# Performance work log

Hardware: AMD Instinct MI355X
Metric: run time of the kernel (lower is better)

## Reference

```python
import jax, jax.numpy as jnp
import numpy as np

B, S, H, V, T, L = 32, 128, 1024, 32000, 100, 4
SD = 0.02


def setup_inputs() -> dict:
    key = jax.random.key(0)
    ks = jax.random.split(key, 20)
    f = jnp.float32
    return {
        "encoder_outputs": jax.random.normal(ks[0], (B, S, H), f),
        "encoder_hidden": jax.random.normal(ks[1], (L, B, H), f),
        "target_tensor": jax.random.randint(ks[2], (B, T), 0, V, dtype=jnp.int32),
        "emb": jax.random.normal(ks[3], (V, H), f) * SD,
        "w_ih0": jax.random.normal(ks[4], (3 * H, 2 * H), f) * SD,
        "w_hh0": jax.random.normal(ks[5], (3 * H, H), f) * SD,
        "b_ih0": jnp.zeros((3 * H,), f),
        "b_hh0": jnp.zeros((3 * H,), f),
        "w_ih": jax.random.normal(ks[6], (L - 1, 3 * H, H), f) * SD,
        "w_hh": jax.random.normal(ks[7], (L - 1, 3 * H, H), f) * SD,
        "b_ih": jnp.zeros((L - 1, 3 * H), f),
        "b_hh": jnp.zeros((L - 1, 3 * H), f),
        "out_w": jax.random.normal(ks[8], (V, H), f) * SD,
        "out_b": jnp.zeros((V,), f),
        "l1_w": jax.random.normal(ks[9], (3, 2 * H), f) * SD,
        "l1_b": jnp.zeros((3,), f),
        "l2_w": jax.random.normal(ks[10], (1, 3), f) * SD,
        "l2_b": jnp.zeros((1,), f),
    }


def _gru_cell(x, h, w_ih, w_hh, b_ih, b_hh):
    # PyTorch GRUCell math
    gi = x @ w_ih.T + b_ih          # [B, 3H]
    gh = h @ w_hh.T + b_hh          # [B, 3H]
    i_r, i_z, i_n = jnp.split(gi, 3, axis=-1)
    h_r, h_z, h_n = jnp.split(gh, 3, axis=-1)
    r = jax.nn.sigmoid(i_r + h_r)
    z = jax.nn.sigmoid(i_z + h_z)
    n = jnp.tanh(i_n + r * h_n)
    return (1.0 - z) * n + z * h


def reference(encoder_outputs, encoder_hidden, target_tensor, emb,
              w_ih0, w_hh0, b_ih0, b_hh0, w_ih, w_hh, b_ih, b_hh,
              out_w, out_b, l1_w, l1_b, l2_w, l2_b):
    b, h = encoder_hidden.shape[1], encoder_hidden.shape[2]
    enc_h = encoder_hidden[0]  # [B, H] 'updated_encoder_hidden'
    # teacher forcing: step 0 uses input 0, step i uses target[:, i-1]
    inputs = jnp.concatenate(
        [jnp.zeros((b, 1), target_tensor.dtype), target_tensor[:, :T - 1]],
        axis=1).T  # [T, B]

    def step(hidden, inp_t):
        # a[:] = hidden[0][-1] -> broadcast last batch row of layer-0 hidden
        a = jnp.broadcast_to(hidden[0, -1], (b, h))
        enc = jnp.concatenate([a, enc_h], axis=1)          # [B, 2H]
        s = (enc @ l1_w.T + l1_b) @ l2_w.T + l2_b          # [B, 1]
        scores = jax.nn.softmax(s, axis=0)                 # softmax over batch dim
        C = jnp.sum(enc_h * scores, axis=0)                # [H]
        e = jax.nn.relu(emb[inp_t])                        # [B, H]
        x = jnp.concatenate([e, jnp.broadcast_to(C, (b, h))], axis=-1)  # [B, 2H]
        h0 = _gru_cell(x, hidden[0], w_ih0, w_hh0, b_ih0, b_hh0)
        hs = [h0]
        xl = h0
        for l in range(L - 1):
            hl = _gru_cell(xl, hidden[l + 1], w_ih[l], w_hh[l], b_ih[l], b_hh[l])
            hs.append(hl)
            xl = hl
        logits = xl @ out_w.T + out_b                      # [B, V]
        return jnp.stack(hs), (logits, scores)

    hidden_fin, (logits, scores) = jax.lax.scan(step, encoder_hidden, inputs)
    dec_out = jax.nn.log_softmax(jnp.transpose(logits, (1, 0, 2)), axis=-1)  # [B, T, V]
    return dec_out, hidden_fin, scores[-1]
```

## Files before the change

### kernel.cpp

```cpp
#include <hip/hip_runtime.h>
#include <hip/hip_bf16.h>
#include <math.h>

#define B_ 32
#define H_ 1024
#define V_ 32000
#define T_ 100
#define L_ 4
#define TB_ (T_*B_)
#define N3H (3*H_)
#define NBLK 224
#define L0BLK 32
#define FSTRIDE 16

typedef __attribute__((ext_vector_type(8))) short bf16x8;
typedef __attribute__((ext_vector_type(4))) float f32x4;
typedef __attribute__((ext_vector_type(4))) unsigned short u16x4;

__device__ inline unsigned short f2bf(float f) {
    union { float f; unsigned u; } v; v.f = f;
    unsigned r = v.u + 0x7fff + ((v.u >> 16) & 1);
    return (unsigned short)(r >> 16);
}
__device__ inline float bf2f(unsigned short u) {
    union { unsigned u; float f; } v; v.u = ((unsigned)u) << 16; return v.f;
}

__device__ inline bf16x8 ld_h16(const unsigned short* p) {
    union { unsigned long long u[2]; bf16x8 v; } r;
    r.u[0] = __hip_atomic_load((const unsigned long long*)p,
                               __ATOMIC_RELAXED, __HIP_MEMORY_SCOPE_AGENT);
    r.u[1] = __hip_atomic_load((const unsigned long long*)(p + 4),
                               __ATOMIC_RELAXED, __HIP_MEMORY_SCOPE_AGENT);
    return r.v;
}
__device__ inline void st_h2(unsigned short* p, unsigned short v) {
    __hip_atomic_store(p, v, __ATOMIC_RELAXED, __HIP_MEMORY_SCOPE_AGENT);
}

__device__ inline void gload_lds16(const unsigned short* g, unsigned short* lds)
{
    __builtin_amdgcn_global_load_lds(
        (const __attribute__((address_space(1))) void*)g,
        (__attribute__((address_space(3))) void*)lds, 16, 0, 0);
}

__global__ __launch_bounds__(256) void convbf_kernel(
    const float* __restrict__ src, unsigned short* __restrict__ dst, int n4)
{
    for (int i = blockIdx.x * 256 + threadIdx.x; i < n4; i += gridDim.x * 256) {
        float4 v = ((const float4*)src)[i];
        u16x4 o; o.x = f2bf(v.x); o.y = f2bf(v.y); o.z = f2bf(v.z); o.w = f2bf(v.w);
        ((u16x4*)dst)[i] = o;
    }
}

__global__ __launch_bounds__(256) void embed_bf_kernel(
    const int* __restrict__ target, const float* __restrict__ emb,
    unsigned short* __restrict__ Ebf)
{
    int bid = blockIdx.x;
    int t = bid >> 5, b = bid & 31;
    int tok = (t == 0) ? 0 : target[b * T_ + (t - 1)];
    float4 v = ((const float4*)(emb + (size_t)tok * H_))[threadIdx.x];
    u16x4 o;
    o.x = f2bf(fmaxf(v.x, 0.f)); o.y = f2bf(fmaxf(v.y, 0.f));
    o.z = f2bf(fmaxf(v.z, 0.f)); o.w = f2bf(fmaxf(v.w, 0.f));
    ((u16x4*)(Ebf + (size_t)bid * H_))[threadIdx.x] = o;
}

__global__ __launch_bounds__(256) void attn_pre_kernel(
    const float* __restrict__ enc_h, const float* __restrict__ l1_w,
    const float* __restrict__ l1_b, const float* __restrict__ l2_w,
    float* __restrict__ Cout, float* __restrict__ scores)
{
    __shared__ float L1h[96];
    __shared__ float sc[32];
    int tid = threadIdx.x, wv = tid >> 6, lane = tid & 63;
    for (int d = wv; d < 96; d += 4) {
        int b = d / 3, g = d - 3 * b;
        const float4* wp = (const float4*)(l1_w + (size_t)g * 2 * H_ + H_);
        const float4* ep = (const float4*)(enc_h + (size_t)b * H_);
        float s = 0.f;
        for (int q = lane; q < 256; q += 64) {
            float4 w4 = wp[q], e4 = ep[q];
            s += w4.x * e4.x + w4.y * e4.y + w4.z * e4.z + w4.w * e4.w;
        }
        for (int o = 32; o > 0; o >>= 1) s += __shfl_down(s, o);
        if (lane == 0) L1h[d] = s;
    }
    __syncthreads();
    if (tid < 32) {
        float cb = 0.f;
        for (int g = 0; g < 3; ++g) cb += l2_w[g] * (L1h[tid * 3 + g] + l1_b[g]);
        sc[tid] = cb;
    }
    __syncthreads();
    if (tid == 0) {
        float m = sc[0];
        for (int b = 1; b < 32; ++b) m = fmaxf(m, sc[b]);
        float s = 0.f;
        for (int b = 0; b < 32; ++b) { float e = expf(sc[b] - m); sc[b] = e; s += e; }
        float inv = 1.f / s;
        for (int b = 0; b < 32; ++b) { sc[b] *= inv; scores[b] = sc[b]; }
    }
    __syncthreads();
    float4 c = make_float4(0.f, 0.f, 0.f, 0.f);
    for (int b = 0; b < 32; ++b) {
        float4 e = ((const float4*)(enc_h + (size_t)b * H_))[tid];
        float ww = sc[b];
        c.x += ww * e.x; c.y += ww * e.y; c.z += ww * e.z; c.w += ww * e.w;
    }
    ((float4*)Cout)[tid] = c;
}

__global__ __launch_bounds__(256) void wcc_kernel(
    const float* __restrict__ w_ih0, const float* __restrict__ C,
    float* __restrict__ wcC)
{
    int row = blockIdx.x * 4 + (threadIdx.x >> 6);
    int lane = threadIdx.x & 63;
    const float4* wp = (const float4*)(w_ih0 + (size_t)row * 2 * H_ + H_);
    const float4* cp = (const float4*)C;
    float s = 0.f;
    for (int q = lane; q < 256; q += 64) {
        float4 w4 = wp[q], c4 = cp[q];
        s += w4.x * c4.x + w4.y * c4.y + w4.z * c4.z + w4.w * c4.w;
    }
    for (int o = 32; o > 0; o >>= 1) s += __shfl_down(s, o);
    if (lane == 0) wcC[row] = s;
}

__global__ __launch_bounds__(256) void gemm_staged(
    const unsigned short* __restrict__ A, int lda,
    const unsigned short* __restrict__ Bb,
    const float* __restrict__ bias, int M, int outMode,
    void* __restrict__ outp)
{
    __shared__ unsigned short Wt[128 * 64];
    __shared__ unsigned short Ht[128 * 64];

    const int tid = threadIdx.x, wv = tid >> 6, lane = tid & 63;
    const int rlo = lane & 15, khw = lane >> 4;
    const int rch = lane >> 3, slot = lane & 7;
    const int rowB = blockIdx.y * 128, colB = blockIdx.x * 128;
    const int wrow0 = rowB + (wv >> 1) * 64;
    const int wcol0 = colB + (wv & 1) * 64;
    const int rA = (wv >> 1) * 64, cA = (wv & 1) * 64;

    f32x4 acc[4][4];
    #pragma unroll
    for (int i = 0; i < 4; ++i)
        #pragma unroll
        for (int j = 0; j < 4; ++j) acc[i][j] = (f32x4){0.f, 0.f, 0.f, 0.f};

    for (int k0 = 0; k0 < H_; k0 += 64) {
        #pragma unroll
        for (int j = 0; j < 4; ++j) {
            int q = wv * 4 + j;
            int row = q * 8 + rch;
            int ss = slot ^ (row & 7);
            gload_lds16(A + (size_t)(rowB + row) * lda + k0 + ss * 8,
                        Wt + (size_t)q * 512);
            gload_lds16(Bb + (size_t)(colB + row) * H_ + k0 + ss * 8,
                        Ht + (size_t)q * 512);
        }
        __syncthreads();

        const char* WtB = (const char*)Wt;
        const char* HtB = (const char*)Ht;
        #pragma unroll
        for (int kk = 0; kk < 2; ++kk) {
            bf16x8 af[4], bfr[4];
            #pragma unroll
            for (int ri = 0; ri < 4; ++ri) {
                int row = rA + ri * 16 + rlo;
                int ch = (kk * 4 + khw) ^ (row & 7);
                af[ri] = *(const bf16x8*)(WtB + row * 128 + ch * 16);
            }
            #pragma unroll
            for (int ci = 0; ci < 4; ++ci) {
                int col = cA + ci * 16 + rlo;
                int ch = (kk * 4 + khw) ^ (col & 7);
                bfr[ci] = *(const bf16x8*)(HtB + col * 128 + ch * 16);
            }
            #pragma unroll
            for (int ri = 0; ri < 4; ++ri)
                #pragma unroll
                for (int ci = 0; ci < 4; ++ci)
                    acc[ri][ci] = __builtin_amdgcn_mfma_f32_16x16x32_bf16(
                        af[ri], bfr[ci], acc[ri][ci], 0, 0, 0);
        }
        __syncthreads();
    }

    int rowoff = (lane >> 4) * 4;
    #pragma unroll
    for (int ri = 0; ri < 4; ++ri) {
        int row = wrow0 + ri * 16 + rowoff;
        float4 bs = *(const float4*)(bias + row);
        #pragma unroll
        for (int ci = 0; ci < 4; ++ci) {
            int col = wcol0 + ci * 16 + rlo;
            float4 v;
            v.x = acc[ri][ci][0] + bs.x; v.y = acc[ri][ci][1] + bs.y;
            v.z = acc[ri][ci][2] + bs.z; v.w = acc[ri][ci][3] + bs.w;
            if (outMode == 1) {
                int tt = col >> 5, b = col & 31;
                *(float4*)((float*)outp + ((size_t)b * T_ + tt) * V_ + row) = v;
            } else {
                u16x4 o; o.x = f2bf(v.x); o.y = f2bf(v.y);
                o.z = f2bf(v.z); o.w = f2bf(v.w);
                *(u16x4*)((unsigned short*)outp + (size_t)col * M + row) = o;
            }
        }
    }
}

__global__ __launch_bounds__(256) void big_gemm_kernel(
    const void* __restrict__ Aptr, int lda, int abf,
    const unsigned short* __restrict__ Bb,
    const float* __restrict__ bias, int M, int outMode,
    void* __restrict__ outp)
{
    int tid = threadIdx.x, wv = tid >> 6, lane = tid & 63;
    int rlo = lane & 15, klane = (lane >> 4) * 8;
    int rowB = blockIdx.y * 128 + (wv >> 1) * 64;
    int colB = blockIdx.x * 128 + (wv & 1) * 64;
    const unsigned short* Ab = (const unsigned short*)Aptr;
    const float* Af = (const float*)Aptr;

    f32x4 acc[4][4];
    #pragma unroll
    for (int i = 0; i < 4; ++i)
        #pragma unroll
        for (int j = 0; j < 4; ++j) acc[i][j] = (f32x4){0.f, 0.f, 0.f, 0.f};

    for (int k0 = 0; k0 < H_; k0 += 32) {
        bf16x8 bfrag[4];
        #pragma unroll
        for (int ci = 0; ci < 4; ++ci) {
            int col = colB + ci * 16 + rlo;
            bfrag[ci] = *(const bf16x8*)(Bb + (size_t)col * H_ + k0 + klane);
        }
        #pragma unroll
        for (int ri = 0; ri < 4; ++ri) {
            int row = rowB + ri * 16 + rlo;
            bf16x8 af;
            if (abf) {
                af = *(const bf16x8*)(Ab + (size_t)row * lda + k0 + klane);
            } else {
                const float* ap = Af + (size_t)row * lda + k0 + klane;
                float4 x0 = *(const float4*)ap, x1 = *(const float4*)(ap + 4);
                af[0] = (short)f2bf(x0.x); af[1] = (short)f2bf(x0.y);
                af[2] = (short)f2bf(x0.z); af[3] = (short)f2bf(x0.w);
                af[4] = (short)f2bf(x1.x); af[5] = (short)f2bf(x1.y);
                af[6] = (short)f2bf(x1.z); af[7] = (short)f2bf(x1.w);
            }
            #pragma unroll
            for (int ci = 0; ci < 4; ++ci)
                acc[ri][ci] = __builtin_amdgcn_mfma_f32_16x16x32_bf16(
                    af, bfrag[ci], acc[ri][ci], 0, 0, 0);
        }
    }

    int rowoff = (lane >> 4) * 4;
    #pragma unroll
    for (int ri = 0; ri < 4; ++ri) {
        int row = rowB + ri * 16 + rowoff;
        float4 bs = *(const float4*)(bias + row);
        #pragma unroll
        for (int ci = 0; ci < 4; ++ci) {
            int col = colB + ci * 16 + rlo;
            float4 v;
            v.x = acc[ri][ci][0] + bs.x; v.y = acc[ri][ci][1] + bs.y;
            v.z = acc[ri][ci][2] + bs.z; v.w = acc[ri][ci][3] + bs.w;
            if (outMode == 1) {
                int tt = col >> 5, b = col & 31;
                *(float4*)((float*)outp + ((size_t)b * T_ + tt) * V_ + row) = v;
            } else {
                u16x4 o; o.x = f2bf(v.x); o.y = f2bf(v.y);
                o.z = f2bf(v.z); o.w = f2bf(v.w);
                *(u16x4*)((unsigned short*)outp + (size_t)col * M + row) = o;
            }
        }
    }
}

__device__ inline void grid_bar4(unsigned* flags, unsigned round)
{
    __syncthreads();
    if (threadIdx.x == 0) {
        asm volatile("s_waitcnt vmcnt(0)" ::: "memory");
        __hip_atomic_store(&flags[(size_t)blockIdx.x * FSTRIDE], round,
                           __ATOMIC_RELAXED, __HIP_MEMORY_SCOPE_AGENT);
    }
    int ok = (threadIdx.x >= NBLK) ? 1 : 0;
    while (true) {
        if (!ok)
            ok = (__hip_atomic_load(&flags[(size_t)threadIdx.x * FSTRIDE],
                                    __ATOMIC_RELAXED, __HIP_MEMORY_SCOPE_AGENT) >= round);
        if (__syncthreads_and(ok)) break;
        __builtin_amdgcn_s_sleep(2);
    }
}

__global__ __launch_bounds__(512, 1) void decode_kernel(
    const unsigned short* __restrict__ whh0_bf,
    const unsigned short* __restrict__ wih_bf,
    const unsigned short* __restrict__ whh_bf,
    const unsigned short* __restrict__ G0,
    const float* __restrict__ b_ih0, const float* __restrict__ b_hh0,
    const float* __restrict__ b_ih,  const float* __restrict__ b_hh,
    const float* __restrict__ enc_hidden,
    unsigned short* __restrict__ hbf,
    unsigned short* __restrict__ Hist,
    float* __restrict__ hid_out,
    unsigned* __restrict__ flags)
{
    __shared__ float sacc[6][4][16][34];
    const int tid = threadIdx.x;
    const int wv = tid >> 6, lane = tid & 63;
    const int rlo = lane & 15, klane = (lane >> 4) * 8;
    const int rowoff = (lane >> 4) * 4;
    const int bid = blockIdx.x;

    int layer, f0;
    if (bid < L0BLK) { layer = 0; f0 = bid << 5; }
    else { int r = bid - L0BLK; layer = 1 + (r >> 6); f0 = (r & 63) << 4; }

    const unsigned short* Wih_l = (layer >= 1) ? wih_bf + (size_t)(layer - 1) * N3H * H_ : nullptr;
    const unsigned short* Whh_l = (layer >= 1) ? whh_bf + (size_t)(layer - 1) * N3H * H_ : whh0_bf;

    const int kc = wv & 3, srcgrp = wv >> 2;

    bf16x8 wreg[3][8];
    int rgv[3];
    #pragma unroll
    for (int i = 0; i < 3; ++i) {
        int rg = srcgrp * 3 + i;
        rgv[i] = rg;
        int wrow; const unsigned short* Wm;
        if (layer == 0)      { wrow = (rg >> 1) * H_ + f0 + (rg & 1) * 16; Wm = Whh_l; }
        else if (rg < 3)     { wrow = rg * H_ + f0;        Wm = Wih_l; }
        else                 { wrow = (rg - 3) * H_ + f0;  Wm = Whh_l; }
        const unsigned short* p = Wm + (size_t)(wrow + rlo) * H_ + kc * 256 + klane;
        #pragma unroll
        for (int s = 0; s < 8; ++s) wreg[i][s] = *(const bf16x8*)(p + s * 32);
    }
    #pragma unroll
    for (int i = 0; i < 3; ++i)
        #pragma unroll
        for (int s = 0; s < 8; ++s)
            asm volatile("" : "+v"(wreg[i][s]));

    const float* bihp = (layer == 0) ? b_ih0 : b_ih + (size_t)(layer - 1) * N3H;
    const float* bhhp = (layer == 0) ? b_hh0 : b_hh + (size_t)(layer - 1) * N3H;
    int jj, eb0;
    float hold0, hold1 = 0.f;
    if (layer == 0) {
        jj = f0 + (tid & 31);
        eb0 = tid >> 5;
        hold0 = enc_hidden[(size_t)eb0 * H_ + jj];
        hold1 = enc_hidden[(size_t)(eb0 + 16) * H_ + jj];
    } else {
        jj = f0 + (tid & 15);
        eb0 = tid >> 4;
        hold0 = enc_hidden[(size_t)layer * B_ * H_ + (size_t)eb0 * H_ + jj];
    }
    const float bir = bihp[jj], biz = bihp[H_ + jj], bin_ = bihp[2 * H_ + jj];
    const float bhr = bhhp[jj], bhz = bhhp[H_ + jj], bhn = bhhp[2 * H_ + jj];

    const size_t BH = (size_t)B_ * H_;

    for (int c = 0; c < T_ + L_ - 1; ++c) {
        int t = c - layer;
        if (t >= 0 && t < T_) {
            int pw = t & 1, pr = pw ^ 1;
            const unsigned short* hown  = hbf + ((size_t)pr * L_ + layer) * BH;
            const unsigned short* hprev = (layer > 0)
                ? hbf + ((size_t)pw * L_ + (layer - 1)) * BH : nullptr;

            f32x4 acc[3][2];
            #pragma unroll
            for (int i = 0; i < 3; ++i) {
                acc[i][0] = (f32x4){0.f, 0.f, 0.f, 0.f};
                acc[i][1] = (f32x4){0.f, 0.f, 0.f, 0.f};
            }

            const unsigned short* hsrc = (layer == 0 || srcgrp == 1) ? hown : hprev;
            const unsigned short* hp = hsrc + (size_t)rlo * H_ + kc * 256 + klane;
            #pragma unroll
            for (int s = 0; s < 8; ++s) {
                bf16x8 b0 = ld_h16(hp + s * 32);
                bf16x8 b1 = ld_h16(hp + 16 * H_ + s * 32);
                #pragma unroll
                for (int i = 0; i < 3; ++i) {
                    acc[i][0] = __builtin_amdgcn_mfma_f32_16x16x32_bf16(wreg[i][s], b0, acc[i][0], 0, 0, 0);
                    acc[i][1] = __builtin_amdgcn_mfma_f32_16x16x32_bf16(wreg[i][s], b1, acc[i][1], 0, 0, 0);
                }
            }

            #pragma unroll
            for (int i = 0; i < 3; ++i)
                #pragma unroll
                for (int r = 0; r < 4; ++r) {
                    sacc[rgv[i]][kc][rowoff + r][rlo]      = acc[i][0][r];
                    sacc[rgv[i]][kc][rowoff + r][16 + rlo] = acc[i][1][r];
                }
            __syncthreads();

            if (layer > 0) {
                int f = tid & 15, b = tid >> 4;
                float ir = bir, iz = biz, in_ = bin_;
                float hr = bhr, hz = bhz, hn = bhn;
                #pragma unroll
                for (int k2 = 0; k2 < 4; ++k2) {
                    ir += sacc[0][k2][f][b]; iz += sacc[1][k2][f][b]; in_ += sacc[2][k2][f][b];
                    hr += sacc[3][k2][f][b]; hz += sacc[4][k2][f][b]; hn += sacc[5][k2][f][b];
                }
                float r = 1.f / (1.f + expf(-(ir + hr)));
                float z = 1.f / (1.f + expf(-(iz + hz)));
                float n = tanhf(in_ + r * hn);
                float hnew = (1.f - z) * n + z * hold0;
                hold0 = hnew;
                unsigned short hb16 = f2bf(hnew);
                st_h2(&hbf[((size_t)pw * L_ + layer) * BH + (size_t)b * H_ + jj], hb16);
                if (layer == L_ - 1) Hist[((size_t)t * B_ + b) * H_ + jj] = hb16;
                if (t == T_ - 1) hid_out[(size_t)layer * BH + (size_t)b * H_ + jj] = hnew;
            } else {
                int fi = tid & 31;
                int rghalf = fi >> 4, fr = fi & 15;
                {
                    int b = eb0;
                    const unsigned short* g0p = G0 + ((size_t)t * B_ + b) * N3H;
                    float ir = bf2f(g0p[jj]) + bir;
                    float iz = bf2f(g0p[H_ + jj]) + biz;
                    float in_ = bf2f(g0p[2 * H_ + jj]) + bin_;
                    float hr = bhr, hz = bhz, hn = bhn;
                    #pragma unroll
                    for (int k2 = 0; k2 < 4; ++k2) {
                        hr += sacc[rghalf][k2][fr][b];
                        hz += sacc[2 + rghalf][k2][fr][b];
                        hn += sacc[4 + rghalf][k2][fr][b];
                    }
                    float r = 1.f / (1.f + expf(-(ir + hr)));
                    float z = 1.f / (1.f + expf(-(iz + hz)));
                    float n = tanhf(in_ + r * hn);
                    float hnew = (1.f - z) * n + z * hold0;
                    hold0 = hnew;
                    st_h2(&hbf[((size_t)pw * L_) * BH + (size_t)b * H_ + jj], f2bf(hnew));
                    if (t == T_ - 1) hid_out[(size_t)b * H_ + jj] = hnew;
                }
                {
                    int b = eb0 + 16;
                    const unsigned short* g0p = G0 + ((size_t)t * B_ + b) * N3H;
                    float ir = bf2f(g0p[jj]) + bir;
                    float iz = bf2f(g0p[H_ + jj]) + biz;
                    float in_ = bf2f(g0p[2 * H_ + jj]) + bin_;
                    float hr = bhr, hz = bhz, hn = bhn;
                    #pragma unroll
                    for (int k2 = 0; k2 < 4; ++k2) {
                        hr += sacc[rghalf][k2][fr][b];
                        hz += sacc[2 + rghalf][k2][fr][b];
                        hn += sacc[4 + rghalf][k2][fr][b];
                    }
                    float r = 1.f / (1.f + expf(-(ir + hr)));
                    float z = 1.f / (1.f + expf(-(iz + hz)));
                    float n = tanhf(in_ + r * hn);
                    float hnew = (1.f - z) * n + z * hold1;
                    hold1 = hnew;
                    st_h2(&hbf[((size_t)pw * L_) * BH + (size_t)b * H_ + jj], f2bf(hnew));
                    if (t == T_ - 1) hid_out[(size_t)b * H_ + jj] = hnew;
                }
            }
        }
        grid_bar4(flags, (unsigned)(c + 1));
    }
}

__global__ __launch_bounds__(256) void logsoftmax_kernel(float* __restrict__ dout)
{
    __shared__ float red[256];
    float4* x4 = (float4*)(dout + (size_t)blockIdx.x * V_);
    const int N4 = V_ / 4;
    int tid = threadIdx.x;

    float m = -INFINITY, s = 0.f;
    for (int i = tid; i < N4; i += 256) {
        float4 v = x4[i];
        float m4 = fmaxf(fmaxf(v.x, v.y), fmaxf(v.z, v.w));
        if (m4 > m) { s *= expf(m - m4); m = m4; }
        s += expf(v.x - m) + expf(v.y - m) + expf(v.z - m) + expf(v.w - m);
    }
    red[tid] = m; __syncthreads();
    for (int o = 128; o > 0; o >>= 1) {
        if (tid < o) red[tid] = fmaxf(red[tid], red[tid + o]);
        __syncthreads();
    }
    float M = red[0]; __syncthreads();
    red[tid] = s * expf(m - M); __syncthreads();
    for (int o = 128; o > 0; o >>= 1) {
        if (tid < o) red[tid] += red[tid + o];
        __syncthreads();
    }
    float lse = M + logf(red[0]);

    for (int i = tid; i < N4; i += 256) {
        float4 v = x4[i];
        v.x -= lse; v.y -= lse; v.z -= lse; v.w -= lse;
        x4[i] = v;
    }
}

extern "C" void kernel_launch(void* const* d_in, const int* in_sizes, int n_in,
                              void* d_out, int out_size, void* d_ws, size_t ws_size,
                              hipStream_t stream)
{
    (void)in_sizes; (void)n_in; (void)out_size;

    const float* enc_hidden = (const float*)d_in[1];
    const int*   target     = (const int*)  d_in[2];
    const float* emb        = (const float*)d_in[3];
    const float* w_ih0      = (const float*)d_in[4];
    const float* w_hh0      = (const float*)d_in[5];
    const float* b_ih0      = (const float*)d_in[6];
    const float* b_hh0      = (const float*)d_in[7];
    const float* w_ih       = (const float*)d_in[8];
    const float* w_hh       = (const float*)d_in[9];
    const float* b_ih       = (const float*)d_in[10];
    const float* b_hh       = (const float*)d_in[11];
    const float* out_w      = (const float*)d_in[12];
    const float* out_b      = (const float*)d_in[13];
    const float* l1_w       = (const float*)d_in[14];
    const float* l1_b       = (const float*)d_in[15];
    const float* l2_w       = (const float*)d_in[16];
    float* out = (float*)d_out;

    char* w = (char*)d_ws;
    auto alloc = [&](size_t bytes) -> char* {
        char* p = w; w += (bytes + 255) & ~(size_t)255; return p;
    };
    unsigned short* whh0_bf = (unsigned short*)alloc((size_t)N3H * H_ * 2);
    unsigned short* wih_bf  = (unsigned short*)alloc((size_t)3 * N3H * H_ * 2);
    unsigned short* whh_bf  = (unsigned short*)alloc((size_t)3 * N3H * H_ * 2);
    unsigned short* Ebf     = (unsigned short*)alloc((size_t)TB_ * H_ * 2);
    unsigned short* G0      = (unsigned short*)alloc((size_t)TB_ * N3H * 2);
    unsigned short* Hist    = (unsigned short*)alloc((size_t)TB_ * H_ * 2);
    unsigned short* hbf     = (unsigned short*)alloc((size_t)2 * L_ * B_ * H_ * 2);
    float*          Cbuf    = (float*)alloc(H_ * 4);
    float*          scores  = (float*)alloc(256);
    float*          wcC     = (float*)alloc(N3H * 4);
    unsigned*       flags   = (unsigned*)alloc((size_t)NBLK * FSTRIDE * 4);

    size_t used = (size_t)(w - (char*)d_ws);
    unsigned short* wih0f_bf = nullptr;
    if (used + (size_t)N3H * 2 * H_ * 2 + 256 <= ws_size)
        wih0f_bf = (unsigned short*)alloc((size_t)N3H * 2 * H_ * 2);
    used = (size_t)(w - (char*)d_ws);
    unsigned short* outw_bf = nullptr;
    if (used + (size_t)V_ * H_ * 2 + 256 <= ws_size)
        outw_bf = (unsigned short*)alloc((size_t)V_ * H_ * 2);

    const size_t LBH = (size_t)L_ * B_ * H_;

    hipMemsetAsync(flags, 0, (size_t)NBLK * FSTRIDE * 4, stream);

    convbf_kernel<<<512, 256, 0, stream>>>(w_hh0, whh0_bf, N3H * H_ / 4);
    convbf_kernel<<<1024, 256, 0, stream>>>(w_ih, wih_bf, 3 * N3H * H_ / 4);
    convbf_kernel<<<1024, 256, 0, stream>>>(w_hh, whh_bf, 3 * N3H * H_ / 4);
    if (wih0f_bf)
        convbf_kernel<<<1024, 256, 0, stream>>>(w_ih0, wih0f_bf, N3H * 2 * H_ / 4);
    if (outw_bf)
        convbf_kernel<<<2048, 256, 0, stream>>>(out_w, outw_bf, V_ * H_ / 4);
    embed_bf_kernel<<<TB_, 256, 0, stream>>>(target, emb, Ebf);
    convbf_kernel<<<128, 256, 0, stream>>>(enc_hidden, hbf + LBH, (int)(LBH / 4));
    attn_pre_kernel<<<1, 256, 0, stream>>>(enc_hidden, l1_w, l1_b, l2_w, Cbuf, scores);
    wcc_kernel<<<N3H / 4, 256, 0, stream>>>(w_ih0, Cbuf, wcC);

    if (wih0f_bf)
        gemm_staged<<<dim3(TB_ / 128, N3H / 128), 256, 0, stream>>>(
            wih0f_bf, 2 * H_, Ebf, wcC, N3H, 0, G0);
    else
        big_gemm_kernel<<<dim3(TB_ / 128, N3H / 128), 256, 0, stream>>>(
            w_ih0, 2 * H_, 0, Ebf, wcC, N3H, 0, G0);

    decode_kernel<<<NBLK, 512, 0, stream>>>(
        whh0_bf, wih_bf, whh_bf, G0, b_ih0, b_hh0, b_ih, b_hh,
        enc_hidden, hbf, Hist, out + (size_t)B_ * T_ * V_, flags);

    if (outw_bf)
        gemm_staged<<<dim3(TB_ / 128, V_ / 128), 256, 0, stream>>>(
            outw_bf, H_, Hist, out_b, V_, 1, out);
    else
        big_gemm_kernel<<<dim3(TB_ / 128, V_ / 128), 256, 0, stream>>>(
            out_w, H_, 0, Hist, out_b, V_, 1, out);
    logsoftmax_kernel<<<TB_, 256, 0, stream>>>(out);

    hipMemcpyAsync(out + (size_t)B_ * T_ * V_ + LBH, scores, B_ * 4,
                   hipMemcpyDeviceToDevice, stream);
}
```

Baseline: 1.851 ms.

## Fuse log-softmax partial stats into output GEMM and store bf16 logits

The vocabulary GEMM epilogue now writes logits as bf16 to a workspace buffer. It also computes a per-tile online max and sum-exp for each column, which a small kernel reduces to a log-sum-exp per (t,b). A streaming subtract kernel then turns the bf16 logits into the final fp32 log-probabilities. The aim is to drop the fp32 logits write and the separate multi-pass log-softmax over the large output, cutting memory traffic. The costs are bf16 rounding of the logits before the subtraction, and the loss of the non-staged fallback GEMM paths.

```diff
diff --git a/kernel.cpp b/kernel.cpp
--- a/kernel.cpp
+++ b/kernel.cpp
@@ -12,10 +12,12 @@
 #define NBLK 224
 #define L0BLK 32
 #define FSTRIDE 16
+#define NVT (V_/128)
 
 typedef __attribute__((ext_vector_type(8))) short bf16x8;
 typedef __attribute__((ext_vector_type(4))) float f32x4;
 typedef __attribute__((ext_vector_type(4))) unsigned short u16x4;
+typedef __attribute__((ext_vector_type(8))) unsigned short u16x8;
 
 __device__ inline unsigned short f2bf(float f) {
     union { float f; unsigned u; } v; v.f = f;
@@ -135,10 +137,11 @@
     const unsigned short* __restrict__ A, int lda,
     const unsigned short* __restrict__ Bb,
     const float* __restrict__ bias, int M, int outMode,
-    void* __restrict__ outp)
+    void* __restrict__ outp, float2* __restrict__ P)
 {
     __shared__ unsigned short Wt[128 * 64];
     __shared__ unsigned short Ht[128 * 64];
+    __shared__ float2 smp[4][4][16];
 
     const int tid = threadIdx.x, wv = tid >> 6, lane = tid & 63;
     const int rlo = lane & 15, khw = lane >> 4;
@@ -195,6 +198,27 @@
     }
 
     int rowoff = (lane >> 4) * 4;
+    if (outMode == 0) {
+        #pragma unroll
+        for (int ri = 0; ri < 4; ++ri) {
+            int row = wrow0 + ri * 16 + rowoff;
+            float4 bs = *(const float4*)(bias + row);
+            #pragma unroll
+            for (int ci = 0; ci < 4; ++ci) {
+                int col = wcol0 + ci * 16 + rlo;
+                u16x4 o;
+                o.x = f2bf(acc[ri][ci][0] + bs.x); o.y = f2bf(acc[ri][ci][1] + bs.y);
+                o.z = f2bf(acc[ri][ci][2] + bs.z); o.w = f2bf(acc[ri][ci][3] + bs.w);
+                *(u16x4*)((unsigned short*)outp + (size_t)col * M + row) = o;
+            }
+        }
+        return;
+    }
+
+    float cm[4], cs[4];
+    #pragma unroll
+    for (int ci = 0; ci < 4; ++ci) { cm[ci] = -INFINITY; cs[ci] = 0.f; }
+    unsigned short* Lbf = (unsigned short*)outp;
     #pragma unroll
     for (int ri = 0; ri < 4; ++ri) {
         int row = wrow0 + ri * 16 + rowoff;
@@ -205,85 +229,70 @@
             float4 v;
             v.x = acc[ri][ci][0] + bs.x; v.y = acc[ri][ci][1] + bs.y;
             v.z = acc[ri][ci][2] + bs.z; v.w = acc[ri][ci][3] + bs.w;
-            if (outMode == 1) {
-                int tt = col >> 5, b = col & 31;
-                *(float4*)((float*)outp + ((size_t)b * T_ + tt) * V_ + row) = v;
-            } else {
-                u16x4 o; o.x = f2bf(v.x); o.y = f2bf(v.y);
-                o.z = f2bf(v.z); o.w = f2bf(v.w);
-                *(u16x4*)((unsigned short*)outp + (size_t)col * M + row) = o;
-            }
-        }
-    }
-}
-
-__global__ __launch_bounds__(256) void big_gemm_kernel(
-    const void* __restrict__ Aptr, int lda, int abf,
-    const unsigned short* __restrict__ Bb,
-    const float* __restrict__ bias, int M, int outMode,
-    void* __restrict__ outp)
-{
-    int tid = threadIdx.x, wv = tid >> 6, lane = tid & 63;
-    int rlo = lane & 15, klane = (lane >> 4) * 8;
-    int rowB = blockIdx.y * 128 + (wv >> 1) * 64;
-    int colB = blockIdx.x * 128 + (wv & 1) * 64;
-    const unsigned short* Ab = (const unsigned short*)Aptr;
-    const float* Af = (const float*)Aptr;
-
-    f32x4 acc[4][4];
-    #pragma unroll
-    for (int i = 0; i < 4; ++i)
-        #pragma unroll
-        for (int j = 0; j < 4; ++j) acc[i][j] = (f32x4){0.f, 0.f, 0.f, 0.f};
-
-    for (int k0 = 0; k0 < H_; k0 += 32) {
-        bf16x8 bfrag[4];
-        #pragma unroll
-        for (int ci = 0; ci < 4; ++ci) {
-            int col = colB + ci * 16 + rlo;
-            bfrag[ci] = *(const bf16x8*)(Bb + (size_t)col * H_ + k0 + klane);
-        }
-        #pragma unroll
-        for (int ri = 0; ri < 4; ++ri) {
-            int row = rowB + ri * 16 + rlo;
-            bf16x8 af;
-            if (abf) {
-                af = *(const bf16x8*)(Ab + (size_t)row * lda + k0 + klane);
-            } else {
-                const float* ap = Af + (size_t)row * lda + k0 + klane;
-                float4 x0 = *(const float4*)ap, x1 = *(const float4*)(ap + 4);
-                af[0] = (short)f2bf(x0.x); af[1] = (short)f2bf(x0.y);
-                af[2] = (short)f2bf(x0.z); af[3] = (short)f2bf(x0.w);
-                af[4] = (short)f2bf(x1.x); af[5] = (short)f2bf(x1.y);
-                af[6] = (short)f2bf(x1.z); af[7] = (short)f2bf(x1.w);
-            }
-            #pragma unroll
-            for (int ci = 0; ci < 4; ++ci)
-                acc[ri][ci] = __builtin_amdgcn_mfma_f32_16x16x32_bf16(
-                    af, bfrag[ci], acc[ri][ci], 0, 0, 0);
-        }
-    }
-
-    int rowoff = (lane >> 4) * 4;
-    #pragma unroll
-    for (int ri = 0; ri < 4; ++ri) {
-        int row = rowB + ri * 16 + rowoff;
-        float4 bs = *(const float4*)(bias + row);
-        #pragma unroll
-        for (int ci = 0; ci < 4; ++ci) {
-            int col = colB + ci * 16 + rlo;
-            float4 v;
-            v.x = acc[ri][ci][0] + bs.x; v.y = acc[ri][ci][1] + bs.y;
-            v.z = acc[ri][ci][2] + bs.z; v.w = acc[ri][ci][3] + bs.w;
-            if (outMode == 1) {
-                int tt = col >> 5, b = col & 31;
-                *(float4*)((float*)outp + ((size_t)b * T_ + tt) * V_ + row) = v;
-            } else {
-                u16x4 o; o.x = f2bf(v.x); o.y = f2bf(v.y);
-                o.z = f2bf(v.z); o.w = f2bf(v.w);
-                *(u16x4*)((unsigned short*)outp + (size_t)col * M + row) = o;
-            }
-        }
+            u16x4 o; o.x = f2bf(v.x); o.y = f2bf(v.y);
+            o.z = f2bf(v.z); o.w = f2bf(v.w);
+            *(u16x4*)(Lbf + (size_t)col * V_ + row) = o;
+            float m4 = fmaxf(fmaxf(v.x, v.y), fmaxf(v.z, v.w));
+            if (m4 > cm[ci]) { cs[ci] *= __expf(cm[ci] - m4); cm[ci] = m4; }
+            cs[ci] += __expf(v.x - cm[ci]) + __expf(v.y - cm[ci])
+                    + __expf(v.z - cm[ci]) + __expf(v.w - cm[ci]);
+        }
+    }
+    #pragma unroll
+    for (int ci = 0; ci < 4; ++ci) {
+        #pragma unroll
+        for (int off = 16; off <= 32; off <<= 1) {
+            float om = __shfl_xor(cm[ci], off);
+            float os = __shfl_xor(cs[ci], off);
+            float mm = fmaxf(cm[ci], om);
+            cs[ci] = cs[ci] * __expf(cm[ci] - mm) + os * __expf(om - mm);
+            cm[ci] = mm;
+        }
+        if ((lane >> 4) == 0) smp[wv][ci][rlo] = make_float2(cm[ci], cs[ci]);
+    }
+    __syncthreads();
+    if (tid < 128) {
+        int c = tid >> 6, ci = (tid >> 4) & 3, rl = tid & 15;
+        float2 a = smp[c][ci][rl], b = smp[c + 2][ci][rl];
+        float mm = fmaxf(a.x, b.x);
+        float ss = a.y * __expf(a.x - mm) + b.y * __expf(b.x - mm);
+        int col = colB + c * 64 + ci * 16 + rl;
+        P[(size_t)blockIdx.y * TB_ + col] = make_float2(mm, ss);
+    }
+}
+
+__global__ __launch_bounds__(256) void lse_finish_kernel(
+    const float2* __restrict__ P, float* __restrict__ lse)
+{
+    int col = blockIdx.x * 256 + threadIdx.x;
+    if (col >= TB_) return;
+    float M = -INFINITY, S = 0.f;
+    for (int i = 0; i < NVT; ++i) {
+        float2 p = P[(size_t)i * TB_ + col];
+        float mm = fmaxf(M, p.x);
+        S = S * __expf(M - mm) + p.y * __expf(p.x - mm);
+        M = mm;
+    }
+    lse[col] = M + logf(S);
+}
+
+__global__ __launch_bounds__(256) void subtract_kernel(
+    const unsigned short* __restrict__ Lbf, const float* __restrict__ lse,
+    float* __restrict__ dout)
+{
+    int col = blockIdx.x;
+    int t = col >> 5, b = col & 31;
+    float l = lse[col];
+    const u16x8* L = (const u16x8*)(Lbf + (size_t)col * V_);
+    float4* o = (float4*)(dout + ((size_t)b * T_ + t) * V_);
+    for (int i = threadIdx.x; i < V_ / 8; i += 256) {
+        u16x8 x = L[i];
+        float4 v0, v1;
+        v0.x = bf2f(x[0]) - l; v0.y = bf2f(x[1]) - l;
+        v0.z = bf2f(x[2]) - l; v0.w = bf2f(x[3]) - l;
+        v1.x = bf2f(x[4]) - l; v1.y = bf2f(x[5]) - l;
+        v1.z = bf2f(x[6]) - l; v1.w = bf2f(x[7]) - l;
+        o[i * 2] = v0; o[i * 2 + 1] = v1;
     }
 }
 
@@ -513,6 +522,80 @@
     }
 }
 
+__global__ __launch_bounds__(256) void gemm_logits_f32(
+    const unsigned short* __restrict__ A,
+    const unsigned short* __restrict__ Bb,
+    const float* __restrict__ bias, float* __restrict__ dout)
+{
+    __shared__ unsigned short Wt[128 * 64];
+    __shared__ unsigned short Ht[128 * 64];
+    const int tid = threadIdx.x, wv = tid >> 6, lane = tid & 63;
+    const int rlo = lane & 15, khw = lane >> 4;
+    const int rch = lane >> 3, slot = lane & 7;
+    const int rowB = blockIdx.y * 128, colB = blockIdx.x * 128;
+    const int wrow0 = rowB + (wv >> 1) * 64;
+    const int wcol0 = colB + (wv & 1) * 64;
+    const int rA = (wv >> 1) * 64, cA = (wv & 1) * 64;
+
+    f32x4 acc[4][4];
+    #pragma unroll
+    for (int i = 0; i < 4; ++i)
+        #pragma unroll
+        for (int j = 0; j < 4; ++j) acc[i][j] = (f32x4){0.f, 0.f, 0.f, 0.f};
+
+    for (int k0 = 0; k0 < H_; k0 += 64) {
+        #pragma unroll
+        for (int j = 0; j < 4; ++j) {
+            int q = wv * 4 + j;
+            int row = q * 8 + rch;
+            int ss = slot ^ (row & 7);
+            gload_lds16(A + (size_t)(rowB + row) * H_ + k0 + ss * 8, Wt + (size_t)q * 512);
+            gload_lds16(Bb + (size_t)(colB + row) * H_ + k0 + ss * 8, Ht + (size_t)q * 512);
+        }
+        __syncthreads();
+        const char* WtB = (const char*)Wt;
+        const char* HtB = (const char*)Ht;
+        #pragma unroll
+        for (int kk = 0; kk < 2; ++kk) {
+            bf16x8 af[4], bfr[4];
+            #pragma unroll
+            for (int ri = 0; ri < 4; ++ri) {
+                int row = rA + ri * 16 + rlo;
+                int ch = (kk * 4 + khw) ^ (row & 7);
+                af[ri] = *(const bf16x8*)(WtB + row * 128 + ch * 16);
+            }
+            #pragma unroll
+            for (int ci = 0; ci < 4; ++ci) {
+                int col = cA + ci * 16 + rlo;
+                int ch = (kk * 4 + khw) ^ (col & 7);
+                bfr[ci] = *(const bf16x8*)(HtB + col * 128 + ch * 16);
+            }
+            #pragma unroll
+            for (int ri = 0; ri < 4; ++ri)
+                #pragma unroll
+                for (int ci = 0; ci < 4; ++ci)
+                    acc[ri][ci] = __builtin_amdgcn_mfma_f32_16x16x32_bf16(
+                        af[ri], bfr[ci], acc[ri][ci], 0, 0, 0);
+        }
+        __syncthreads();
+    }
+    int rowoff = (lane >> 4) * 4;
+    #pragma unroll
+    for (int ri = 0; ri < 4; ++ri) {
+        int row = wrow0 + ri * 16 + rowoff;
+        float4 bs = *(const float4*)(bias + row);
+        #pragma unroll
+        for (int ci = 0; ci < 4; ++ci) {
+            int col = wcol0 + ci * 16 + rlo;
+            int tt = col >> 5, b = col & 31;
+            float4 v;
+            v.x = acc[ri][ci][0] + bs.x; v.y = acc[ri][ci][1] + bs.y;
+            v.z = acc[ri][ci][2] + bs.z; v.w = acc[ri][ci][3] + bs.w;
+            *(float4*)(dout + ((size_t)b * T_ + tt) * V_ + row) = v;
+        }
+    }
+}
+
 extern "C" void kernel_launch(void* const* d_in, const int* in_sizes, int n_in,
                               void* d_out, int out_size, void* d_ws, size_t ws_size,
                               hipStream_t stream)
@@ -552,6 +635,8 @@
     float*          scores  = (float*)alloc(256);
     float*          wcC     = (float*)alloc(N3H * 4);
     unsigned*       flags   = (unsigned*)alloc((size_t)NBLK * FSTRIDE * 4);
+    float2*         Ppart   = (float2*)alloc((size_t)NVT * TB_ * 8);
+    float*          lse     = (float*)alloc((size_t)TB_ * 4);
 
     size_t used = (size_t)(w - (char*)d_ws);
     unsigned short* wih0f_bf = nullptr;
@@ -561,6 +646,10 @@
     unsigned short* outw_bf = nullptr;
     if (used + (size_t)V_ * H_ * 2 + 256 <= ws_size)
         outw_bf = (unsigned short*)alloc((size_t)V_ * H_ * 2);
+    used = (size_t)(w - (char*)d_ws);
+    unsigned short* Lbf = nullptr;
+    if (used + (size_t)TB_ * V_ * 2 + 256 <= ws_size)
+        Lbf = (unsigned short*)alloc((size_t)TB_ * V_ * 2);
 
     const size_t LBH = (size_t)L_ * B_ * H_;
 
@@ -578,24 +667,23 @@
     attn_pre_kernel<<<1, 256, 0, stream>>>(enc_hidden, l1_w, l1_b, l2_w, Cbuf, scores);
     wcc_kernel<<<N3H / 4, 256, 0, stream>>>(w_ih0, Cbuf, wcC);
 
-    if (wih0f_bf)
-        gemm_staged<<<dim3(TB_ / 128, N3H / 128), 256, 0, stream>>>(
-            wih0f_bf, 2 * H_, Ebf, wcC, N3H, 0, G0);
-    else
-        big_gemm_kernel<<<dim3(TB_ / 128, N3H / 128), 256, 0, stream>>>(
-            w_ih0, 2 * H_, 0, Ebf, wcC, N3H, 0, G0);
+    gemm_staged<<<dim3(TB_ / 128, N3H / 128), 256, 0, stream>>>(
+        wih0f_bf, 2 * H_, Ebf, wcC, N3H, 0, G0, nullptr);
 
     decode_kernel<<<NBLK, 512, 0, stream>>>(
         whh0_bf, wih_bf, whh_bf, G0, b_ih0, b_hh0, b_ih, b_hh,
         enc_hidden, hbf, Hist, out + (size_t)B_ * T_ * V_, flags);
 
-    if (outw_bf)
+    if (outw_bf && Lbf) {
         gemm_staged<<<dim3(TB_ / 128, V_ / 128), 256, 0, stream>>>(
-            outw_bf, H_, Hist, out_b, V_, 1, out);
-    else
-        big_gemm_kernel<<<dim3(TB_ / 128, V_ / 128), 256, 0, stream>>>(
-            out_w, H_, 0, Hist, out_b, V_, 1, out);
-    logsoftmax_kernel<<<TB_, 256, 0, stream>>>(out);
+            outw_bf, H_, Hist, out_b, V_, 2, Lbf, Ppart);
+        lse_finish_kernel<<<(TB_ + 255) / 256, 256, 0, stream>>>(Ppart, lse);
+        subtract_kernel<<<TB_, 256, 0, stream>>>(Lbf, lse, out);
+    } else if (outw_bf) {
+        gemm_logits_f32<<<dim3(TB_ / 128, V_ / 128), 256, 0, stream>>>(
+            outw_bf, Hist, out_b, out);
+        logsoftmax_kernel<<<TB_, 256, 0, stream>>>(out);
+    }
 
     hipMemcpyAsync(out + (size_t)B_ * T_ * V_ + LBH, scores, B_ * 4,
                    hipMemcpyDeviceToDevice, stream);
```

Result: no change. 1.821 ms (-1.6%).
